# Performance work log

Hardware: AMD Instinct MI355X
Metric: run time of the kernel (lower is better)

## Reference

```python
import jax, jax.numpy as jnp
import numpy as np

B, S, IN, HID, OUT = 32, 512, 256, 512, 256
CTX = IN + 2 * HID


def _glorot(key, shape):
    lim = np.sqrt(6.0 / (shape[0] + shape[-1])) if len(shape) > 1 else np.sqrt(6.0 / shape[0])
    return jax.random.uniform(key, shape, jnp.float32, -lim, lim)


def setup_inputs() -> dict:
    key = jax.random.key(0)
    ks = jax.random.split(key, 12)
    inp = {
        "x": jax.random.normal(ks[0], (B, S, IN), jnp.float32),
        # forward GRU cell (TF GRUCell param layout: [x,h] @ W)
        "fw_Wg": _glorot(ks[1], (IN + HID, 2 * HID)),
        "fw_bg": jnp.ones((2 * HID,), jnp.float32),  # TF GRU gate bias init = 1.0
        "fw_Wc": _glorot(ks[2], (IN + HID, HID)),
        "fw_bc": jnp.zeros((HID,), jnp.float32),
        # backward GRU cell
        "bw_Wg": _glorot(ks[3], (IN + HID, 2 * HID)),
        "bw_bg": jnp.ones((2 * HID,), jnp.float32),
        "bw_Wc": _glorot(ks[4], (IN + HID, HID)),
        "bw_bc": jnp.zeros((HID,), jnp.float32),
        # FC over shifted-context concat, then MLP head
        "fc_w": _glorot(ks[5], (CTX, HID)),
        "fc_b": _glorot(ks[6], (HID,)),
        "mlp_w": _glorot(ks[7], (HID, OUT)),
        "mlp_b": jnp.zeros((OUT,), jnp.float32),
    }
    return inp


def _gru(x_sbd, Wg, bg, Wc, bc):
    """x_sbd: [S,B,IN] -> outputs [S,B,HID]. TF GRUCell math."""
    h0 = jnp.zeros((x_sbd.shape[1], Wc.shape[1]), x_sbd.dtype)

    def step(h, xt):
        ru = jax.nn.sigmoid(jnp.concatenate([xt, h], -1) @ Wg + bg)
        r, u = jnp.split(ru, 2, axis=-1)
        c = jnp.tanh(jnp.concatenate([xt, r * h], -1) @ Wc + bc)
        h_new = u * h + (1.0 - u) * c
        return h_new, h_new

    _, ys = jax.lax.scan(step, h0, x_sbd)
    return ys


def reference(x, fw_Wg, fw_bg, fw_Wc, fw_bc, bw_Wg, bw_bg, bw_Wc, bw_bc, fc_w, fc_b, mlp_w, mlp_b):
    x_sbd = jnp.transpose(x, (1, 0, 2))  # [S,B,IN]
    out_fw = jnp.transpose(_gru(x_sbd, fw_Wg, fw_bg, fw_Wc, fw_bc), (1, 0, 2))  # [B,S,H]
    out_bw_rev = _gru(x_sbd[::-1], bw_Wg, bw_bg, bw_Wc, bw_bc)
    out_bw = jnp.transpose(out_bw_rev[::-1], (1, 0, 2))  # [B,S,H], time-aligned

    zero = jnp.zeros((x.shape[0], 1, out_fw.shape[2]), x.dtype)
    c_left = jnp.concatenate([zero, out_fw[:, :-1]], axis=1)
    c_right = jnp.concatenate([out_bw[:, 1:], zero], axis=1)
    last = jnp.concatenate([c_left, x, c_right], axis=2)  # [B,S,CTX]

    fc_lin = jax.nn.relu(jnp.einsum('bsc,ch->bsh', last, fc_w) + fc_b)
    fc_pool = jnp.max(fc_lin, axis=1)  # [B,H]
    return fc_pool @ mlp_w + mlp_b  # [B,OUT]
```

## Files before the change

### kernel.cpp

```cpp
#include <hip/hip_runtime.h>
#include <hip/hip_bf16.h>
#include <cstdint>
#include <cstddef>

#define B_    32
#define S_    512
#define IN_   256
#define HID_  512
#define NGATE 1024
#define OUT_  256
#define NWGD  16
#define STP   536

typedef float f32x4 __attribute__((ext_vector_type(4)));
typedef short bf16x8 __attribute__((ext_vector_type(8)));
typedef unsigned long long ull;

__device__ inline unsigned short f2bf(float f) {
  return __builtin_bit_cast(unsigned short, __float2bfloat16(f));
}
__device__ inline float bf2f(unsigned short u) {
  union { float f; unsigned int i; } v; v.i = ((unsigned int)u) << 16; return v.f;
}

__device__ inline void store_short_cc(unsigned short* p, unsigned short val, bool fast) {
  unsigned v = val;
  if (fast) asm volatile("global_store_short %0, %1, off sc0"     :: "v"(p), "v"(v) : "memory");
  else      asm volatile("global_store_short %0, %1, off sc0 sc1" :: "v"(p), "v"(v) : "memory");
}
__device__ inline void store_dword_wt(unsigned* p, unsigned val) {
  asm volatile("global_store_dword %0, %1, off sc0 sc1" :: "v"(p), "v"(val) : "memory");
}
__device__ inline void store_dword_l2(unsigned* p, unsigned val) {
  asm volatile("global_store_dword %0, %1, off sc0" :: "v"(p), "v"(val) : "memory");
}

__global__ void prep_kernel(const float* __restrict__ x,
                            const float* __restrict__ fcw,
                            unsigned short* __restrict__ Xbf,
                            unsigned short* __restrict__ HFW,
                            unsigned short* __restrict__ HBW,
                            float* __restrict__ pool,
                            unsigned* __restrict__ sync,
                            unsigned short* __restrict__ fcwf)
{
  const int nthreads = gridDim.x * blockDim.x;
  const int gtid = blockIdx.x * blockDim.x + threadIdx.x;

  for (int i = gtid; i < S_*B_*IN_; i += nthreads) {
    int c = i & (IN_-1);
    int rem = i >> 8;
    int b = rem & (B_-1);
    int s = rem >> 5;
    Xbf[((size_t)s*B_ + b)*IN_ + c] = f2bf(x[((size_t)b*S_ + s)*IN_ + c]);
  }
  for (int i = gtid; i < B_*HID_; i += nthreads) {
    HFW[i] = 0;
    HBW[(size_t)(S_-1)*B_*HID_ + i] = 0;
  }
  for (int i = gtid; i < B_*HID_; i += nthreads) pool[i] = 0.f;
  for (int i = gtid; i < 4096;    i += nthreads) sync[i] = 0u;
  for (int i = gtid; i < 40*32*64*8; i += nthreads) {
    int j     = i & 7;
    int lane_ = (i >> 3) & 63;
    int nt    = (i >> 9) & 31;
    int kc    = i >> 14;
    int k = kc*32 + (lane_ >> 4)*8 + j;
    int n = nt*16 + (lane_ & 15);
    fcwf[i] = f2bf(fcw[(size_t)k*HID_ + n]);
  }
}

__global__ __launch_bounds__(256, 1)
void pregemm_kernel(const unsigned short* __restrict__ Xbf,
                    const float* __restrict__ Wg_fw, const float* __restrict__ bg_fw,
                    const float* __restrict__ Wc_fw, const float* __restrict__ bc_fw,
                    const float* __restrict__ Wg_bw, const float* __restrict__ bg_bw,
                    const float* __restrict__ Wc_bw, const float* __restrict__ bc_bw,
                    unsigned short* __restrict__ GX, unsigned short* __restrict__ GC)
{
  __shared__ unsigned short bsm[4*8*64*8];
  const int id  = blockIdx.x;
  const int dir = id >= 6144;
  const int r0  = id - dir*6144;
  const int mtile = r0 / 24;
  const int sec   = r0 % 24;
  const bool isG  = sec < 16;
  const float* W    = dir ? (isG ? Wg_bw : Wc_bw) : (isG ? Wg_fw : Wc_fw);
  const float* bias = dir ? (isG ? bg_bw : bc_bw) : (isG ? bg_fw : bc_fw);
  const int N     = isG ? NGATE : HID_;
  const int nbase = (isG ? sec : sec - 16) * 64;
  unsigned short* out = isG ? (GX + (size_t)dir*16384*NGATE)
                            : (GC + (size_t)dir*16384*HID_);
  const int m0 = mtile * 64;
  const int tid = threadIdx.x, wave = tid >> 6, lane = tid & 63;
  const int quad = lane >> 4, l16 = lane & 15;

  for (int idx = tid; idx < 4*8*64; idx += 256) {
    int lane_ = idx & 63, kk = (idx >> 6) & 7, nt = idx >> 9;
    int n  = nbase + nt*16 + (lane_ & 15);
    int kb = kk*32 + (lane_ >> 4)*8;
    #pragma unroll
    for (int j = 0; j < 8; ++j)
      bsm[((nt*8 + kk)*64 + lane_)*8 + j] = f2bf(W[(size_t)(kb + j)*N + n]);
  }
  __syncthreads();

  f32x4 acc[4];
  #pragma unroll
  for (int nt = 0; nt < 4; ++nt) acc[nt] = (f32x4){0.f,0.f,0.f,0.f};
  #pragma unroll
  for (int kk = 0; kk < 8; ++kk) {
    bf16x8 af = *(const bf16x8*)(Xbf + (size_t)(m0 + wave*16 + l16)*IN_ + quad*8 + kk*32);
    #pragma unroll
    for (int nt = 0; nt < 4; ++nt) {
      bf16x8 bv = *(const bf16x8*)(&bsm[((nt*8 + kk)*64 + lane)*8]);
      acc[nt] = __builtin_amdgcn_mfma_f32_16x16x32_bf16(af, bv, acc[nt], 0, 0, 0);
    }
  }
  #pragma unroll
  for (int nt = 0; nt < 4; ++nt)
    #pragma unroll
    for (int r = 0; r < 4; ++r) {
      int row = m0 + wave*16 + quad*4 + r;
      int col = nbase + nt*16 + l16;
      out[(size_t)row*N + col] = f2bf(acc[nt][r] + bias[col]);
    }
}

__device__ inline void wait_flags2(const unsigned* basef, const unsigned* bases,
                                   unsigned target, bool fast) {
  const int fi = threadIdx.x & (NWGD-1);
  if (fast) {
    const volatile unsigned* pf = basef + fi*16;
    const unsigned* ps = bases + fi*16;
    int it = 0;
    for (;;) {
      asm volatile("buffer_inv sc0" ::: "memory");
      unsigned v = *pf;
      if (!__any((int)(v < target))) return;
      if ((++it & 31) == 0) {
        unsigned w = __hip_atomic_load(ps, __ATOMIC_RELAXED, __HIP_MEMORY_SCOPE_AGENT);
        if (!__any((int)(w < target))) return;
      }
      __builtin_amdgcn_s_sleep(1);
    }
  } else {
    const unsigned* ps = bases + fi*16;
    for (;;) {
      unsigned v = __hip_atomic_load(ps, __ATOMIC_RELAXED, __HIP_MEMORY_SCOPE_AGENT);
      if (!__any((int)(v < target))) return;
      __builtin_amdgcn_s_sleep(1);
    }
  }
}

__global__ __launch_bounds__(512, 1)
void gru_kernel(const float* __restrict__ Wg_fw, const float* __restrict__ Wc_fw,
                const float* __restrict__ Wg_bw, const float* __restrict__ Wc_bw,
                const unsigned short* __restrict__ GX, const unsigned short* __restrict__ GC,
                unsigned short* __restrict__ HFW, unsigned short* __restrict__ HBW,
                unsigned short* __restrict__ RH, unsigned* __restrict__ sync)
{
  __shared__ __align__(16) unsigned short wg_lds[4][16][512];
  __shared__ __align__(16) unsigned short wc_lds[2][16][512];
  __shared__ __align__(16) unsigned short st_lds[32*STP];
  __shared__ float u_lds[32][32];

  const int slot = blockIdx.x & 7;
  if (slot >= 2) return;
  const int dir = slot;
  const int g   = blockIdx.x >> 3;
  const int tid = threadIdx.x;
  const int wave = tid >> 6, lane = tid & 63;
  const int quad = lane >> 4, l16 = lane & 15;

  const float* Wg = dir ? Wg_bw : Wg_fw;
  const float* Wc = dir ? Wc_bw : Wc_fw;
  unsigned short* H = dir ? HBW : HFW;
  unsigned short* RHd = RH + (size_t)dir*S_*B_*HID_;
  const unsigned short* GXd = GX + (size_t)dir*16384*NGATE;
  const unsigned short* GCd = GC + (size_t)dir*16384*HID_;
  unsigned* fAf = sync + dir*1024;
  unsigned* fBf = sync + dir*1024 + 256;
  unsigned* fAs = sync + dir*1024 + 512;
  unsigned* fBs = sync + dir*1024 + 768;

  {
    unsigned xcc = __builtin_amdgcn_s_getreg((31 << 11) | (0 << 6) | 20);
    if (tid == 0) store_dword_wt(sync + 2048 + dir*64 + g*4, 0x100u | (xcc & 0xFu));
  }

  for (int idx = tid; idx < 4*16*64; idx += 512) {
    int lane_ = idx & 63, kk = (idx >> 6) & 15, nt = idx >> 10;
    int l16_ = lane_ & 15;
    int n = (nt < 2) ? (g*32 + nt*16 + l16_) : (512 + g*32 + (nt-2)*16 + l16_);
    int kb = IN_ + kk*32 + (lane_ >> 4)*8;
    #pragma unroll
    for (int j = 0; j < 8; ++j)
      wg_lds[nt][kk][lane_*8 + j] = f2bf(Wg[(size_t)(kb + j)*NGATE + n]);
  }
  for (int idx = tid; idx < 2*16*64; idx += 512) {
    int lane_ = idx & 63, kk = (idx >> 6) & 15, nt = idx >> 10;
    int n  = g*32 + nt*16 + (lane_ & 15);
    int kb = IN_ + kk*32 + (lane_ >> 4)*8;
    #pragma unroll
    for (int j = 0; j < 8; ++j)
      wc_lds[nt][kk][lane_*8 + j] = f2bf(Wc[(size_t)(kb + j)*HID_ + n]);
  }
  __syncthreads();

  bool fast;
  {
    const unsigned* p = sync + 2048 + dir*64 + (tid & 15)*4;
    unsigned v;
    for (;;) {
      v = __hip_atomic_load(p, __ATOMIC_RELAXED, __HIP_MEMORY_SCOPE_AGENT);
      if (!__any((int)((v & 0x100u) == 0u))) break;
      __builtin_amdgcn_s_sleep(1);
    }
    unsigned v0 = __shfl(v, 0, 64);
    fast = (__all((int)(v == v0)) != 0);
  }

  const int amt = wave >> 2, ant = wave & 3;
  const int b0A = amt*16 + quad*4;
  const int bmt = wave & 1, bnt = (wave >> 1) & 1;
  const int b0B = bmt*16 + quad*4;
  const int colB = g*32 + bnt*16 + l16;
  const int colg = (ant < 2) ? (g*32 + ant*16 + l16)
                             : (512 + g*32 + (ant-2)*16 + l16);

  for (int si = 0; si < S_; ++si) {
    const int t  = dir ? (S_-1-si) : si;
    const int to = dir ? (t-1)     : (t+1);

    unsigned short gx_s[4], gc_s[4];
    {
      const unsigned short* gx = GXd + (size_t)t*B_*NGATE;
      #pragma unroll
      for (int r = 0; r < 4; ++r) gx_s[r] = gx[(size_t)(b0A + r)*NGATE + colg];
      if (wave < 4) {
        #pragma unroll
        for (int r = 0; r < 4; ++r)
          gc_s[r] = GCd[((size_t)t*B_ + b0B + r)*HID_ + colB];
      }
    }

    wait_flags2(fBf, fBs, (unsigned)si, fast);

    {
      const uint4* src = (const uint4*)(H + (size_t)t*B_*HID_);
      #pragma unroll
      for (int i = 0; i < 4; ++i) {
        int c = tid + i*512;
        int row = c >> 6, col8 = c & 63;
        *(uint4*)&st_lds[row*STP + col8*8] = src[c];
      }
    }
    __syncthreads();

    float gcv[4], hpB[4];
    {
      float gxv[4];
      #pragma unroll
      for (int r = 0; r < 4; ++r) gxv[r] = bf2f(gx_s[r]);
      float hpA[4];
      if (ant < 2) {
        #pragma unroll
        for (int r = 0; r < 4; ++r) hpA[r] = bf2f(st_lds[(b0A + r)*STP + colg]);
      }
      if (wave < 4) {
        #pragma unroll
        for (int r = 0; r < 4; ++r) {
          gcv[r] = bf2f(gc_s[r]);
          hpB[r] = bf2f(st_lds[(b0B + r)*STP + colB]);
        }
      }
      f32x4 a0 = {0.f,0.f,0.f,0.f}, a1 = {0.f,0.f,0.f,0.f};
      #pragma unroll
      for (int kk = 0; kk < 16; ++kk) {
        bf16x8 af = *(const bf16x8*)(&st_lds[(amt*16 + l16)*STP + quad*8 + kk*32]);
        bf16x8 bv = *(const bf16x8*)(&wg_lds[ant][kk][lane*8]);
        if (kk & 1) a1 = __builtin_amdgcn_mfma_f32_16x16x32_bf16(af, bv, a1, 0, 0, 0);
        else        a0 = __builtin_amdgcn_mfma_f32_16x16x32_bf16(af, bv, a0, 0, 0, 0);
      }
      f32x4 acc = a0 + a1;
      if (ant < 2) {
        #pragma unroll
        for (int r = 0; r < 4; ++r) {
          float rv = 1.f / (1.f + __expf(-(acc[r] + gxv[r])));
          store_short_cc(&RHd[(size_t)t*B_*HID_ + (size_t)(b0A + r)*HID_ + colg],
                         f2bf(rv * hpA[r]), fast);
        }
      } else {
        #pragma unroll
        for (int r = 0; r < 4; ++r)
          u_lds[b0A + r][(ant-2)*16 + l16] = 1.f / (1.f + __expf(-(acc[r] + gxv[r])));
      }
    }
    __syncthreads();
    if (tid == 0) {
      if (fast) store_dword_l2(fAf + g*16, (unsigned)(si + 1));
      store_dword_wt(fAs + g*16, (unsigned)(si + 1));
    }

    wait_flags2(fAf, fAs, (unsigned)(si + 1), fast);
    {
      const uint4* src = (const uint4*)(RHd + (size_t)t*B_*HID_);
      #pragma unroll
      for (int i = 0; i < 4; ++i) {
        int c = tid + i*512;
        int row = c >> 6, col8 = c & 63;
        *(uint4*)&st_lds[row*STP + col8*8] = src[c];
      }
    }
    __syncthreads();

    if (wave < 4) {
      f32x4 a0 = {0.f,0.f,0.f,0.f}, a1 = {0.f,0.f,0.f,0.f};
      #pragma unroll
      for (int kk = 0; kk < 16; ++kk) {
        bf16x8 af = *(const bf16x8*)(&st_lds[(bmt*16 + l16)*STP + quad*8 + kk*32]);
        bf16x8 bv = *(const bf16x8*)(&wc_lds[bnt][kk][lane*8]);
        if (kk & 1) a1 = __builtin_amdgcn_mfma_f32_16x16x32_bf16(af, bv, a1, 0, 0, 0);
        else        a0 = __builtin_amdgcn_mfma_f32_16x16x32_bf16(af, bv, a0, 0, 0, 0);
      }
      f32x4 acc = a0 + a1;
      if (to >= 0 && to < S_) {
        #pragma unroll
        for (int r = 0; r < 4; ++r) {
          float c  = tanhf(acc[r] + gcv[r]);
          float u  = u_lds[b0B + r][bnt*16 + l16];
          float hn = u * hpB[r] + (1.f - u)*c;
          store_short_cc(&H[((size_t)to*B_ + b0B + r)*HID_ + colB], f2bf(hn), fast);
        }
      }
    }
    __syncthreads();
    if (tid == 0) {
      if (fast) store_dword_l2(fBf + g*16, (unsigned)(si + 1));
      store_dword_wt(fBs + g*16, (unsigned)(si + 1));
    }
  }
}

__global__ __launch_bounds__(512, 1)
void fc_kernel(const unsigned short* __restrict__ HFW, const unsigned short* __restrict__ HBW,
               const unsigned short* __restrict__ Xbf,
               const unsigned short* __restrict__ fcwf, const float* __restrict__ fcb,
               float* __restrict__ pool)
{
  __shared__ unsigned short bsm[32*512];
  __shared__ float red[8*512];
  const int wg = blockIdx.x;
  const int b  = wg >> 2;
  const int tid = threadIdx.x, wave = tid >> 6, lane = tid & 63;
  const int quad = lane >> 4, l16 = lane & 15;
  const int t = (wg & 3)*128 + wave*16 + l16;

  f32x4 acc[32];
  #pragma unroll
  for (int nt = 0; nt < 32; ++nt) acc[nt] = (f32x4){0.f,0.f,0.f,0.f};

  for (int kc = 0; kc < 40; ++kc) {
    __syncthreads();
    const uint4* src = (const uint4*)(fcwf + (size_t)kc*32*512);
    uint4* dst = (uint4*)bsm;
    #pragma unroll
    for (int r = 0; r < 4; ++r) dst[tid + r*512] = src[tid + r*512];
    __syncthreads();

    const unsigned short* ap;
    if (kc < 16)      ap = HFW + ((size_t)t*B_ + b)*HID_ + kc*32 + quad*8;
    else if (kc < 24) ap = Xbf + ((size_t)t*B_ + b)*IN_ + (kc - 16)*32 + quad*8;
    else              ap = HBW + ((size_t)t*B_ + b)*HID_ + (kc - 24)*32 + quad*8;
    const bf16x8 af = *(const bf16x8*)ap;
    #pragma unroll
    for (int nt = 0; nt < 32; ++nt) {
      bf16x8 bfv = *(const bf16x8*)(&bsm[(nt*64 + lane)*8]);
      acc[nt] = __builtin_amdgcn_mfma_f32_16x16x32_bf16(af, bfv, acc[nt], 0, 0, 0);
    }
  }
  #pragma unroll
  for (int nt = 0; nt < 32; ++nt) {
    float m = fmaxf(fmaxf(acc[nt][0], acc[nt][1]), fmaxf(acc[nt][2], acc[nt][3]));
    m = fmaxf(m, __shfl_xor(m, 16, 64));
    m = fmaxf(m, __shfl_xor(m, 32, 64));
    if (quad == 0) red[wave*512 + nt*16 + l16] = m;
  }
  __syncthreads();
  {
    float m = red[tid];
    #pragma unroll
    for (int w = 1; w < 8; ++w) m = fmaxf(m, red[w*512 + tid]);
    m = fmaxf(m + fcb[tid], 0.f);
    atomicMax((int*)&pool[(size_t)b*HID_ + tid], __float_as_int(m));
  }
}

__global__ void mlp_kernel(const float* __restrict__ pool, const float* __restrict__ w,
                           const float* __restrict__ bias, float* __restrict__ out)
{
  __shared__ float p[HID_];
  const int b = blockIdx.x, tid = threadIdx.x;
  p[tid]       = pool[(size_t)b*HID_ + tid];
  p[tid + 256] = pool[(size_t)b*HID_ + 256 + tid];
  __syncthreads();
  float acc = bias[tid];
  for (int k = 0; k < HID_; ++k) acc += p[k] * w[(size_t)k*OUT_ + tid];
  out[(size_t)b*OUT_ + tid] = acc;
}

extern "C" void kernel_launch(void* const* d_in, const int* in_sizes, int n_in,
                              void* d_out, int out_size, void* d_ws, size_t ws_size,
                              hipStream_t stream)
{
  const float* x    = (const float*)d_in[0];
  const float* fwWg = (const float*)d_in[1];
  const float* fwbg = (const float*)d_in[2];
  const float* fwWc = (const float*)d_in[3];
  const float* fwbc = (const float*)d_in[4];
  const float* bwWg = (const float*)d_in[5];
  const float* bwbg = (const float*)d_in[6];
  const float* bwWc = (const float*)d_in[7];
  const float* bwbc = (const float*)d_in[8];
  const float* fcw  = (const float*)d_in[9];
  const float* fcb  = (const float*)d_in[10];
  const float* mlpw = (const float*)d_in[11];
  const float* mlpb = (const float*)d_in[12];
  float* out = (float*)d_out;

  char* p = (char*)d_ws;
  auto take = [&](size_t bytes) { char* r = p; p += (bytes + 255) & ~size_t(255); return r; };
  unsigned short* Xbf  = (unsigned short*)take((size_t)S_*B_*IN_*2);
  unsigned short* HFW  = (unsigned short*)take((size_t)S_*B_*HID_*2);
  unsigned short* HBW  = (unsigned short*)take((size_t)S_*B_*HID_*2);
  unsigned short* GX   = (unsigned short*)take((size_t)2*S_*B_*NGATE*2);
  unsigned short* GC   = (unsigned short*)take((size_t)2*S_*B_*HID_*2);
  unsigned short* RH   = (unsigned short*)take((size_t)2*S_*B_*HID_*2);
  unsigned short* fcwf = (unsigned short*)take((size_t)40*32*64*8*2);
  float*          pool = (float*)take((size_t)B_*HID_*4);
  unsigned*       sync = (unsigned*)take(16384);

  prep_kernel<<<2048, 256, 0, stream>>>(x, fcw, Xbf, HFW, HBW, pool, sync, fcwf);
  pregemm_kernel<<<12288, 256, 0, stream>>>(Xbf, fwWg, fwbg, fwWc, fwbc,
                                            bwWg, bwbg, bwWc, bwbc, GX, GC);
  gru_kernel<<<128, 512, 0, stream>>>(fwWg, fwWc, bwWg, bwWc,
                                      GX, GC, HFW, HBW, RH, sync);
  fc_kernel<<<128, 512, 0, stream>>>(HFW, HBW, Xbf, fcwf, fcb, pool);
  mlp_kernel<<<32, 256, 0, stream>>>(pool, mlpw, mlpb, out);
}
```

Baseline: 2.494 ms.

## Split recurrent state wait and GEMM into two K-halves to overlap sync

The per-step cross-workgroup wait is split into two halves. Each workgroup waits only on the eight producers of one half of the hidden or reset-state columns, loads that half into a double-buffered LDS tile, and runs its partial MFMA accumulation before waiting on the other half. This lets compute on the first half overlap with producers still writing the second half. The s_sleep in the fast spin loop is also removed to cut polling latency, at the cost of heavier memory polling traffic and an extra __syncthreads per half.

```diff
diff --git a/kernel.cpp b/kernel.cpp
--- a/kernel.cpp
+++ b/kernel.cpp
@@ -10,7 +10,7 @@
 #define NGATE 1024
 #define OUT_  256
 #define NWGD  16
-#define STP   536
+#define STW   264
 
 typedef float f32x4 __attribute__((ext_vector_type(4)));
 typedef short bf16x8 __attribute__((ext_vector_type(8)));
@@ -128,9 +128,9 @@
     }
 }
 
-__device__ inline void wait_flags2(const unsigned* basef, const unsigned* bases,
-                                   unsigned target, bool fast) {
-  const int fi = threadIdx.x & (NWGD-1);
+__device__ inline void wait_half(const unsigned* basef, const unsigned* bases,
+                                 unsigned target, bool fast, int hf) {
+  const int fi = hf*8 + (threadIdx.x & 7);
   if (fast) {
     const volatile unsigned* pf = basef + fi*16;
     const unsigned* ps = bases + fi*16;
@@ -143,7 +143,6 @@
         unsigned w = __hip_atomic_load(ps, __ATOMIC_RELAXED, __HIP_MEMORY_SCOPE_AGENT);
         if (!__any((int)(w < target))) return;
       }
-      __builtin_amdgcn_s_sleep(1);
     }
   } else {
     const unsigned* ps = bases + fi*16;
@@ -164,7 +163,7 @@
 {
   __shared__ __align__(16) unsigned short wg_lds[4][16][512];
   __shared__ __align__(16) unsigned short wc_lds[2][16][512];
-  __shared__ __align__(16) unsigned short st_lds[32*STP];
+  __shared__ __align__(16) unsigned short st_lds[2][32][STW];
   __shared__ float u_lds[32][32];
 
   const int slot = blockIdx.x & 7;
@@ -230,10 +229,15 @@
   const int colB = g*32 + bnt*16 + l16;
   const int colg = (ant < 2) ? (g*32 + ant*16 + l16)
                              : (512 + g*32 + (ant-2)*16 + l16);
+  const int ghalf = g >> 3;
+  const int clA = (g*32 + ((ant < 2) ? ant : 0)*16 + l16) & 255;
+  const int clB = colB & 255;
 
   for (int si = 0; si < S_; ++si) {
     const int t  = dir ? (S_-1-si) : si;
     const int to = dir ? (t-1)     : (t+1);
+    const unsigned short* Hsrc  = H   + (size_t)t*B_*HID_;
+    const unsigned short* RHsrc = RHd + (size_t)t*B_*HID_;
 
     unsigned short gx_s[4], gc_s[4];
     {
@@ -247,56 +251,52 @@
       }
     }
 
-    wait_flags2(fBf, fBs, (unsigned)si, fast);
-
+    float hpA[4], hpB[4], gcv[4];
+    f32x4 a0 = {0.f,0.f,0.f,0.f}, a1 = {0.f,0.f,0.f,0.f};
+    #pragma unroll
+    for (int hf = 0; hf < 2; ++hf) {
+      wait_half(fBf, fBs, (unsigned)si, fast, hf);
+      {
+        const uint4* src = (const uint4*)Hsrc;
+        #pragma unroll
+        for (int i = 0; i < 2; ++i) {
+          int c = tid + i*512;
+          int row = c >> 5, c16 = c & 31;
+          *(uint4*)&st_lds[hf][row][c16*8] = src[row*64 + hf*32 + c16];
+        }
+      }
+      __syncthreads();
+      if (hf == ghalf) {
+        if (ant < 2) {
+          #pragma unroll
+          for (int r = 0; r < 4; ++r) hpA[r] = bf2f(st_lds[hf][b0A + r][clA]);
+        }
+        if (wave < 4) {
+          #pragma unroll
+          for (int r = 0; r < 4; ++r) hpB[r] = bf2f(st_lds[hf][b0B + r][clB]);
+        }
+      }
+      #pragma unroll
+      for (int kkl = 0; kkl < 8; ++kkl) {
+        bf16x8 af = *(const bf16x8*)(&st_lds[hf][amt*16 + l16][quad*8 + kkl*32]);
+        bf16x8 bv = *(const bf16x8*)(&wg_lds[ant][hf*8 + kkl][lane*8]);
+        if (kkl & 1) a1 = __builtin_amdgcn_mfma_f32_16x16x32_bf16(af, bv, a1, 0, 0, 0);
+        else         a0 = __builtin_amdgcn_mfma_f32_16x16x32_bf16(af, bv, a0, 0, 0, 0);
+      }
+    }
     {
-      const uint4* src = (const uint4*)(H + (size_t)t*B_*HID_);
-      #pragma unroll
-      for (int i = 0; i < 4; ++i) {
-        int c = tid + i*512;
-        int row = c >> 6, col8 = c & 63;
-        *(uint4*)&st_lds[row*STP + col8*8] = src[c];
-      }
-    }
-    __syncthreads();
-
-    float gcv[4], hpB[4];
-    {
-      float gxv[4];
-      #pragma unroll
-      for (int r = 0; r < 4; ++r) gxv[r] = bf2f(gx_s[r]);
-      float hpA[4];
-      if (ant < 2) {
-        #pragma unroll
-        for (int r = 0; r < 4; ++r) hpA[r] = bf2f(st_lds[(b0A + r)*STP + colg]);
-      }
-      if (wave < 4) {
-        #pragma unroll
-        for (int r = 0; r < 4; ++r) {
-          gcv[r] = bf2f(gc_s[r]);
-          hpB[r] = bf2f(st_lds[(b0B + r)*STP + colB]);
-        }
-      }
-      f32x4 a0 = {0.f,0.f,0.f,0.f}, a1 = {0.f,0.f,0.f,0.f};
-      #pragma unroll
-      for (int kk = 0; kk < 16; ++kk) {
-        bf16x8 af = *(const bf16x8*)(&st_lds[(amt*16 + l16)*STP + quad*8 + kk*32]);
-        bf16x8 bv = *(const bf16x8*)(&wg_lds[ant][kk][lane*8]);
-        if (kk & 1) a1 = __builtin_amdgcn_mfma_f32_16x16x32_bf16(af, bv, a1, 0, 0, 0);
-        else        a0 = __builtin_amdgcn_mfma_f32_16x16x32_bf16(af, bv, a0, 0, 0, 0);
-      }
       f32x4 acc = a0 + a1;
       if (ant < 2) {
         #pragma unroll
         for (int r = 0; r < 4; ++r) {
-          float rv = 1.f / (1.f + __expf(-(acc[r] + gxv[r])));
+          float rv = 1.f / (1.f + __expf(-(acc[r] + bf2f(gx_s[r]))));
           store_short_cc(&RHd[(size_t)t*B_*HID_ + (size_t)(b0A + r)*HID_ + colg],
                          f2bf(rv * hpA[r]), fast);
         }
       } else {
         #pragma unroll
         for (int r = 0; r < 4; ++r)
-          u_lds[b0A + r][(ant-2)*16 + l16] = 1.f / (1.f + __expf(-(acc[r] + gxv[r])));
+          u_lds[b0A + r][(ant-2)*16 + l16] = 1.f / (1.f + __expf(-(acc[r] + bf2f(gx_s[r]))));
       }
     }
     __syncthreads();
@@ -305,36 +305,38 @@
       store_dword_wt(fAs + g*16, (unsigned)(si + 1));
     }
 
-    wait_flags2(fAf, fAs, (unsigned)(si + 1), fast);
-    {
-      const uint4* src = (const uint4*)(RHd + (size_t)t*B_*HID_);
+    f32x4 c0 = {0.f,0.f,0.f,0.f}, c1 = {0.f,0.f,0.f,0.f};
+    #pragma unroll
+    for (int hf = 0; hf < 2; ++hf) {
+      wait_half(fAf, fAs, (unsigned)(si + 1), fast, hf);
+      {
+        const uint4* src = (const uint4*)RHsrc;
+        #pragma unroll
+        for (int i = 0; i < 2; ++i) {
+          int c = tid + i*512;
+          int row = c >> 5, c16 = c & 31;
+          *(uint4*)&st_lds[hf][row][c16*8] = src[row*64 + hf*32 + c16];
+        }
+      }
+      __syncthreads();
+      if (wave < 4) {
+        #pragma unroll
+        for (int kkl = 0; kkl < 8; ++kkl) {
+          bf16x8 af = *(const bf16x8*)(&st_lds[hf][bmt*16 + l16][quad*8 + kkl*32]);
+          bf16x8 bv = *(const bf16x8*)(&wc_lds[bnt][hf*8 + kkl][lane*8]);
+          if (kkl & 1) c1 = __builtin_amdgcn_mfma_f32_16x16x32_bf16(af, bv, c1, 0, 0, 0);
+          else         c0 = __builtin_amdgcn_mfma_f32_16x16x32_bf16(af, bv, c0, 0, 0, 0);
+        }
+      }
+    }
+    if (wave < 4 && to >= 0 && to < S_) {
+      f32x4 acc = c0 + c1;
       #pragma unroll
-      for (int i = 0; i < 4; ++i) {
-        int c = tid + i*512;
-        int row = c >> 6, col8 = c & 63;
-        *(uint4*)&st_lds[row*STP + col8*8] = src[c];
-      }
-    }
-    __syncthreads();
-
-    if (wave < 4) {
-      f32x4 a0 = {0.f,0.f,0.f,0.f}, a1 = {0.f,0.f,0.f,0.f};
-      #pragma unroll
-      for (int kk = 0; kk < 16; ++kk) {
-        bf16x8 af = *(const bf16x8*)(&st_lds[(bmt*16 + l16)*STP + quad*8 + kk*32]);
-        bf16x8 bv = *(const bf16x8*)(&wc_lds[bnt][kk][lane*8]);
-        if (kk & 1) a1 = __builtin_amdgcn_mfma_f32_16x16x32_bf16(af, bv, a1, 0, 0, 0);
-        else        a0 = __builtin_amdgcn_mfma_f32_16x16x32_bf16(af, bv, a0, 0, 0, 0);
-      }
-      f32x4 acc = a0 + a1;
-      if (to >= 0 && to < S_) {
-        #pragma unroll
-        for (int r = 0; r < 4; ++r) {
-          float c  = tanhf(acc[r] + gcv[r]);
-          float u  = u_lds[b0B + r][bnt*16 + l16];
-          float hn = u * hpB[r] + (1.f - u)*c;
-          store_short_cc(&H[((size_t)to*B_ + b0B + r)*HID_ + colB], f2bf(hn), fast);
-        }
+      for (int r = 0; r < 4; ++r) {
+        float c  = tanhf(acc[r] + bf2f(gc_s[r]));
+        float u  = u_lds[b0B + r][bnt*16 + l16];
+        float hn = u * hpB[r] + (1.f - u)*c;
+        store_short_cc(&H[((size_t)to*B_ + b0B + r)*HID_ + colB], f2bf(hn), fast);
       }
     }
     __syncthreads();
```

New measurement: 2.993 ms. 20.0% more time.

## Remap GRU recurrence to 4 waves, each computing r, u and candidate for its tile

Applied to the files above, without the earlier changes.

Shrinks the GRU workgroup from 8 to 4 waves. Each wave now owns one 16x16 output tile and computes both the reset and update gate MFMAs for it, then the candidate MFMA. The update gate stays in registers instead of passing through shared memory, and all waves do work in the candidate phase. The cost is that each wave runs twice as many gate MFMAs and twice as many state-copy loads, which lengthens the serial per-step critical path in a latency-bound recurrence.

```diff
diff --git a/kernel.cpp b/kernel.cpp
--- a/kernel.cpp
+++ b/kernel.cpp
@@ -155,7 +155,7 @@
   }
 }
 
-__global__ __launch_bounds__(512, 1)
+__global__ __launch_bounds__(256, 1)
 void gru_kernel(const float* __restrict__ Wg_fw, const float* __restrict__ Wc_fw,
                 const float* __restrict__ Wg_bw, const float* __restrict__ Wc_bw,
                 const unsigned short* __restrict__ GX, const unsigned short* __restrict__ GC,
@@ -165,7 +165,6 @@
   __shared__ __align__(16) unsigned short wg_lds[4][16][512];
   __shared__ __align__(16) unsigned short wc_lds[2][16][512];
   __shared__ __align__(16) unsigned short st_lds[32*STP];
-  __shared__ float u_lds[32][32];
 
   const int slot = blockIdx.x & 7;
   if (slot >= 2) return;
@@ -191,7 +190,7 @@
     if (tid == 0) store_dword_wt(sync + 2048 + dir*64 + g*4, 0x100u | (xcc & 0xFu));
   }
 
-  for (int idx = tid; idx < 4*16*64; idx += 512) {
+  for (int idx = tid; idx < 4*16*64; idx += 256) {
     int lane_ = idx & 63, kk = (idx >> 6) & 15, nt = idx >> 10;
     int l16_ = lane_ & 15;
     int n = (nt < 2) ? (g*32 + nt*16 + l16_) : (512 + g*32 + (nt-2)*16 + l16_);
@@ -200,7 +199,7 @@
     for (int j = 0; j < 8; ++j)
       wg_lds[nt][kk][lane_*8 + j] = f2bf(Wg[(size_t)(kb + j)*NGATE + n]);
   }
-  for (int idx = tid; idx < 2*16*64; idx += 512) {
+  for (int idx = tid; idx < 2*16*64; idx += 256) {
     int lane_ = idx & 63, kk = (idx >> 6) & 15, nt = idx >> 10;
     int n  = g*32 + nt*16 + (lane_ & 15);
     int kb = IN_ + kk*32 + (lane_ >> 4)*8;
@@ -223,27 +222,23 @@
     fast = (__all((int)(v == v0)) != 0);
   }
 
-  const int amt = wave >> 2, ant = wave & 3;
-  const int b0A = amt*16 + quad*4;
-  const int bmt = wave & 1, bnt = (wave >> 1) & 1;
-  const int b0B = bmt*16 + quad*4;
-  const int colB = g*32 + bnt*16 + l16;
-  const int colg = (ant < 2) ? (g*32 + ant*16 + l16)
-                             : (512 + g*32 + (ant-2)*16 + l16);
+  const int mt = wave & 1, nc = wave >> 1;
+  const int b0 = mt*16 + quad*4;
+  const int colr = g*32 + nc*16 + l16;
+  const int colu = 512 + colr;
 
   for (int si = 0; si < S_; ++si) {
     const int t  = dir ? (S_-1-si) : si;
     const int to = dir ? (t-1)     : (t+1);
 
-    unsigned short gx_s[4], gc_s[4];
+    unsigned short gxr_s[4], gxu_s[4], gc_s[4];
     {
       const unsigned short* gx = GXd + (size_t)t*B_*NGATE;
       #pragma unroll
-      for (int r = 0; r < 4; ++r) gx_s[r] = gx[(size_t)(b0A + r)*NGATE + colg];
-      if (wave < 4) {
-        #pragma unroll
-        for (int r = 0; r < 4; ++r)
-          gc_s[r] = GCd[((size_t)t*B_ + b0B + r)*HID_ + colB];
+      for (int r = 0; r < 4; ++r) {
+        gxr_s[r] = gx[(size_t)(b0 + r)*NGATE + colr];
+        gxu_s[r] = gx[(size_t)(b0 + r)*NGATE + colu];
+        gc_s[r]  = GCd[((size_t)t*B_ + b0 + r)*HID_ + colr];
       }
     }
 
@@ -252,51 +247,40 @@
     {
       const uint4* src = (const uint4*)(H + (size_t)t*B_*HID_);
       #pragma unroll
-      for (int i = 0; i < 4; ++i) {
-        int c = tid + i*512;
+      for (int i = 0; i < 8; ++i) {
+        int c = tid + i*256;
         int row = c >> 6, col8 = c & 63;
         *(uint4*)&st_lds[row*STP + col8*8] = src[c];
       }
     }
     __syncthreads();
 
-    float gcv[4], hpB[4];
+    float hp[4], uv[4];
     {
-      float gxv[4];
-      #pragma unroll
-      for (int r = 0; r < 4; ++r) gxv[r] = bf2f(gx_s[r]);
-      float hpA[4];
-      if (ant < 2) {
-        #pragma unroll
-        for (int r = 0; r < 4; ++r) hpA[r] = bf2f(st_lds[(b0A + r)*STP + colg]);
-      }
-      if (wave < 4) {
-        #pragma unroll
-        for (int r = 0; r < 4; ++r) {
-          gcv[r] = bf2f(gc_s[r]);
-          hpB[r] = bf2f(st_lds[(b0B + r)*STP + colB]);
+      #pragma unroll
+      for (int r = 0; r < 4; ++r) hp[r] = bf2f(st_lds[(b0 + r)*STP + colr]);
+      f32x4 a0 = {0.f,0.f,0.f,0.f}, a1 = {0.f,0.f,0.f,0.f};
+      f32x4 u0 = {0.f,0.f,0.f,0.f}, u1 = {0.f,0.f,0.f,0.f};
+      #pragma unroll
+      for (int kk = 0; kk < 16; ++kk) {
+        bf16x8 af  = *(const bf16x8*)(&st_lds[(mt*16 + l16)*STP + quad*8 + kk*32]);
+        bf16x8 bvr = *(const bf16x8*)(&wg_lds[nc][kk][lane*8]);
+        bf16x8 bvu = *(const bf16x8*)(&wg_lds[2 + nc][kk][lane*8]);
+        if (kk & 1) {
+          a1 = __builtin_amdgcn_mfma_f32_16x16x32_bf16(af, bvr, a1, 0, 0, 0);
+          u1 = __builtin_amdgcn_mfma_f32_16x16x32_bf16(af, bvu, u1, 0, 0, 0);
+        } else {
+          a0 = __builtin_amdgcn_mfma_f32_16x16x32_bf16(af, bvr, a0, 0, 0, 0);
+          u0 = __builtin_amdgcn_mfma_f32_16x16x32_bf16(af, bvu, u0, 0, 0, 0);
         }
       }
-      f32x4 a0 = {0.f,0.f,0.f,0.f}, a1 = {0.f,0.f,0.f,0.f};
-      #pragma unroll
-      for (int kk = 0; kk < 16; ++kk) {
-        bf16x8 af = *(const bf16x8*)(&st_lds[(amt*16 + l16)*STP + quad*8 + kk*32]);
-        bf16x8 bv = *(const bf16x8*)(&wg_lds[ant][kk][lane*8]);
-        if (kk & 1) a1 = __builtin_amdgcn_mfma_f32_16x16x32_bf16(af, bv, a1, 0, 0, 0);
-        else        a0 = __builtin_amdgcn_mfma_f32_16x16x32_bf16(af, bv, a0, 0, 0, 0);
-      }
-      f32x4 acc = a0 + a1;
-      if (ant < 2) {
-        #pragma unroll
-        for (int r = 0; r < 4; ++r) {
-          float rv = 1.f / (1.f + __expf(-(acc[r] + gxv[r])));
-          store_short_cc(&RHd[(size_t)t*B_*HID_ + (size_t)(b0A + r)*HID_ + colg],
-                         f2bf(rv * hpA[r]), fast);
-        }
-      } else {
-        #pragma unroll
-        for (int r = 0; r < 4; ++r)
-          u_lds[b0A + r][(ant-2)*16 + l16] = 1.f / (1.f + __expf(-(acc[r] + gxv[r])));
+      f32x4 racc = a0 + a1, uacc = u0 + u1;
+      #pragma unroll
+      for (int r = 0; r < 4; ++r) {
+        float rv = 1.f / (1.f + __expf(-(racc[r] + bf2f(gxr_s[r]))));
+        store_short_cc(&RHd[(size_t)t*B_*HID_ + (size_t)(b0 + r)*HID_ + colr],
+                       f2bf(rv * hp[r]), fast);
+        uv[r] = 1.f / (1.f + __expf(-(uacc[r] + bf2f(gxu_s[r]))));
       }
     }
     __syncthreads();
@@ -309,31 +293,30 @@
     {
       const uint4* src = (const uint4*)(RHd + (size_t)t*B_*HID_);
       #pragma unroll
-      for (int i = 0; i < 4; ++i) {
-        int c = tid + i*512;
+      for (int i = 0; i < 8; ++i) {
+        int c = tid + i*256;
         int row = c >> 6, col8 = c & 63;
         *(uint4*)&st_lds[row*STP + col8*8] = src[c];
       }
     }
     __syncthreads();
 
-    if (wave < 4) {
-      f32x4 a0 = {0.f,0.f,0.f,0.f}, a1 = {0.f,0.f,0.f,0.f};
+    {
+      f32x4 c0 = {0.f,0.f,0.f,0.f}, c1 = {0.f,0.f,0.f,0.f};
       #pragma unroll
       for (int kk = 0; kk < 16; ++kk) {
-        bf16x8 af = *(const bf16x8*)(&st_lds[(bmt*16 + l16)*STP + quad*8 + kk*32]);
-        bf16x8 bv = *(const bf16x8*)(&wc_lds[bnt][kk][lane*8]);
-        if (kk & 1) a1 = __builtin_amdgcn_mfma_f32_16x16x32_bf16(af, bv, a1, 0, 0, 0);
-        else        a0 = __builtin_amdgcn_mfma_f32_16x16x32_bf16(af, bv, a0, 0, 0, 0);
-      }
-      f32x4 acc = a0 + a1;
+        bf16x8 af = *(const bf16x8*)(&st_lds[(mt*16 + l16)*STP + quad*8 + kk*32]);
+        bf16x8 bv = *(const bf16x8*)(&wc_lds[nc][kk][lane*8]);
+        if (kk & 1) c1 = __builtin_amdgcn_mfma_f32_16x16x32_bf16(af, bv, c1, 0, 0, 0);
+        else        c0 = __builtin_amdgcn_mfma_f32_16x16x32_bf16(af, bv, c0, 0, 0, 0);
+      }
+      f32x4 cacc = c0 + c1;
       if (to >= 0 && to < S_) {
         #pragma unroll
         for (int r = 0; r < 4; ++r) {
-          float c  = tanhf(acc[r] + gcv[r]);
-          float u  = u_lds[b0B + r][bnt*16 + l16];
-          float hn = u * hpB[r] + (1.f - u)*c;
-          store_short_cc(&H[((size_t)to*B_ + b0B + r)*HID_ + colB], f2bf(hn), fast);
+          float c  = tanhf(cacc[r] + bf2f(gc_s[r]));
+          float hn = uv[r] * hp[r] + (1.f - uv[r]) * c;
+          store_short_cc(&H[((size_t)to*B_ + b0 + r)*HID_ + colr], f2bf(hn), fast);
         }
       }
     }
@@ -446,7 +429,7 @@
   prep_kernel<<<2048, 256, 0, stream>>>(x, fcw, Xbf, HFW, HBW, pool, sync, fcwf);
   pregemm_kernel<<<12288, 256, 0, stream>>>(Xbf, fwWg, fwbg, fwWc, fwbc,
                                             bwWg, bwbg, bwWc, bwbc, GX, GC);
-  gru_kernel<<<128, 512, 0, stream>>>(fwWg, fwWc, bwWg, bwWc,
+  gru_kernel<<<128, 256, 0, stream>>>(fwWg, fwWc, bwWg, bwWc,
                                       GX, GC, HFW, HBW, RH, sync);
   fc_kernel<<<128, 512, 0, stream>>>(HFW, HBW, Xbf, fcwf, fcb, pool);
   mlp_kernel<<<32, 256, 0, stream>>>(pool, mlpw, mlpb, out);
```

Result: faster. 2.396 ms (-3.9%).
